# Kernel tuning notes

Hardware: AMD Instinct MI355X
Metric: run time of the kernel (lower is better)

## Reference

```python
import jax, jax.numpy as jnp
import numpy as np

DIM = 768
HEADS = 12
HEAD_DIM = DIM // HEADS
SCALE = HEAD_DIM ** (-0.5)


def setup_inputs() -> dict:
    key = jax.random.key(0)
    k1, k2, k3 = jax.random.split(key, 3)
    x = jax.random.normal(k1, (4, 2048, DIM), dtype=jnp.float32)
    # nn.Linear(dim, 3*dim, bias=False): weight [3*dim, dim]
    w_qkv = jax.random.normal(k2, (3 * DIM, DIM), dtype=jnp.float32) * (DIM ** -0.5)
    # nn.Linear(dim, dim) with bias
    w_proj = jax.random.normal(k3, (DIM, DIM), dtype=jnp.float32) * (DIM ** -0.5)
    b_proj = jnp.zeros((DIM,), dtype=jnp.float32)
    return {"x": x, "w_qkv": w_qkv, "w_proj": w_proj, "b_proj": b_proj}


def reference(x, w_qkv, w_proj, b_proj):
    B, N, C = x.shape
    H, D = HEADS, HEAD_DIM
    qkv = jnp.einsum('bnc,oc->bno', x, w_qkv)  # [B,N,3C]
    qkv = qkv.reshape(B, N, 3, H, D).transpose(2, 0, 3, 1, 4)  # [3,B,H,N,D]
    q, k, v = qkv[0], qkv[1], qkv[2]
    attn = jnp.einsum('bhnd,bhmd->bhnm', q, k) * SCALE  # [B,H,N,N]
    attn = jax.nn.softmax(attn, axis=-1)
    attn = jax.nn.softmax(attn, axis=-1)  # double softmax, as in original
    out = jnp.einsum('bhnm,bhmd->bhnd', attn, v)  # [B,H,N,D]
    out = out.transpose(0, 2, 1, 3).reshape(B, N, C)
    return jnp.einsum('bnc,oc->bno', out, w_proj) + b_proj
```

## Files before the change

### kernel.cpp

```cpp
#include <hip/hip_runtime.h>
#include <hip/hip_bf16.h>

#define DIM 768
#define HEADS 12
#define HD 64
#define SEQ 2048
#define BATCH 4
#define BHN 48
#define TOK 8192

#if __has_builtin(__builtin_amdgcn_exp2f)
#define EXP2F __builtin_amdgcn_exp2f
#else
#define EXP2F exp2f
#endif
#define EXP_C 0.1803368801111244f

using short8  = __attribute__((ext_vector_type(8))) short;
using short4v = __attribute__((ext_vector_type(4))) short;
using float4v = __attribute__((ext_vector_type(4))) float;

__device__ __forceinline__ short f2b(float f) {
    union { float f; unsigned u; } v; v.f = f;
    unsigned r = v.u + 0x7FFF + ((v.u >> 16) & 1);
    return (short)(r >> 16);
}
__device__ __forceinline__ float b2f(short s) {
    union { unsigned u; float f; } v;
    v.u = ((unsigned)(unsigned short)s) << 16;
    return v.f;
}
__device__ __forceinline__ unsigned pk2(float a, float b) {
    union { float f; unsigned u; } x, y; x.f = a; y.f = b;
    return __builtin_amdgcn_perm(x.u + 0x8000u, y.u + 0x8000u, 0x03020706u);
}

typedef const __attribute__((address_space(1))) unsigned GU;
typedef __attribute__((address_space(3))) unsigned LU;
__device__ __forceinline__ void gload_lds16(const short* g, short* l) {
    __builtin_amdgcn_global_load_lds((GU*)g, (LU*)l, 16, 0, 0);
}

__global__ void cast_all(const float* __restrict__ x, const float* __restrict__ wq,
                         const float* __restrict__ wp,
                         short* __restrict__ xb, short* __restrict__ wqb,
                         short* __restrict__ wpb, float* __restrict__ Vsum,
                         int nx4, int nq4) {
    int i = blockIdx.x * 256 + threadIdx.x;
    if (i < BHN * 64) Vsum[i] = 0.f;
    const float* in; short* out; int j = i;
    if (i < nx4)            { in = x;  out = xb;  }
    else if (i < nx4 + nq4) { in = wq; out = wqb; j = i - nx4; }
    else                    { in = wp; out = wpb; j = i - nx4 - nq4; }
    float4 f = ((const float4*)in)[j];
    short4 o;
    o.x = f2b(f.x); o.y = f2b(f.y); o.z = f2b(f.z); o.w = f2b(f.w);
    ((short4*)out)[j] = o;
}

__global__ __launch_bounds__(256, 4)
void gemm_qkv(const short* __restrict__ A, const short* __restrict__ Bw,
              short* __restrict__ Qw, short* __restrict__ Kw, short* __restrict__ Vw,
              float* __restrict__ Vsum)
{
    __shared__ __align__(16) short As[2][128 * 32];
    __shared__ __align__(16) short Bs[2][128 * 32];

    const int tid  = threadIdx.x;
    const int lane = tid & 63;
    const int wave = tid >> 6;
    const int wm = (wave >> 1) * 64, wn = (wave & 1) * 64;
    const int l15 = lane & 15, quad = lane >> 4;

    const int gid = blockIdx.x;
    const int w   = gid >> 3;
    const int ybl = (gid & 7) * 8 + (w & 7);
    const int xbl = w >> 3;

    const bool vpart = (xbl >= 12);
    const short* rowsP = vpart ? (Bw + 1536 * 768) : A;
    const short* colsP = vpart ? A : Bw;
    const int m0 = vpart ? (xbl - 12) * 128 : ybl * 128;
    const int n0 = vpart ? ybl * 128 : xbl * 128;
    const int K = DIM;

    float4v acc[4][4];
    #pragma unroll
    for (int i = 0; i < 4; i++)
        #pragma unroll
        for (int j = 0; j < 4; j++)
            acc[i][j] = (float4v){0.f, 0.f, 0.f, 0.f};

    const int G0 = wave * 128 + lane;
    const int G1 = G0 + 64;
    const int rA0 = G0 >> 2, cA0 = (G0 & 3) * 8;
    const int rA1 = G1 >> 2, cA1 = (G1 & 3) * 8;
    const int ldsoff = wave * 1024;

    for (int kt = 0; kt < K; kt += 64) {
        #pragma unroll
        for (int s = 0; s < 2; s++) {
            const int kc = kt + s * 32;
            gload_lds16(&rowsP[(size_t)(m0 + rA0) * K + kc + cA0], &As[s][ldsoff]);
            gload_lds16(&rowsP[(size_t)(m0 + rA1) * K + kc + cA1], &As[s][ldsoff + 512]);
            gload_lds16(&colsP[(size_t)(n0 + rA0) * K + kc + cA0], &Bs[s][ldsoff]);
            gload_lds16(&colsP[(size_t)(n0 + rA1) * K + kc + cA1], &Bs[s][ldsoff + 512]);
        }
        __syncthreads();
        #pragma unroll
        for (int s = 0; s < 2; s++) {
            short8 af[4], bfr[4];
            #pragma unroll
            for (int t = 0; t < 4; t++) {
                af[t]  = *(const short8*)&As[s][(wm + t * 16 + l15) * 32 + quad * 8];
                bfr[t] = *(const short8*)&Bs[s][(wn + t * 16 + l15) * 32 + quad * 8];
            }
            #pragma unroll
            for (int tm = 0; tm < 4; tm++)
                #pragma unroll
                for (int tn = 0; tn < 4; tn++)
                    acc[tm][tn] = __builtin_amdgcn_mfma_f32_16x16x32_bf16(af[tm], bfr[tn], acc[tm][tn], 0, 0, 0);
        }
        __syncthreads();
    }

    #pragma unroll
    for (int tm = 0; tm < 4; tm++)
        #pragma unroll
        for (int tn = 0; tn < 4; tn++)
            #pragma unroll
            for (int r = 0; r < 4; r++) {
                int row = m0 + wm + tm * 16 + quad * 4 + r;
                int col = n0 + wn + tn * 16 + l15;
                float v = acc[tm][tn][r];
                if (vpart) {
                    int hh = row >> 6, d = row & 63;
                    int b = col >> 11, n = col & 2047;
                    int bh = b * HEADS + hh;
                    int t2 = n >> 6, c2h = (n >> 5) & 1, wk = n & 31;
                    int slot = ((wk & 15) >> 2) * 8 + ((wk & 16) >> 2) + (wk & 3);
                    int g2 = c2h * 4 + (slot >> 3);
                    int gp2 = g2 ^ (d & 7);
                    Vw[(size_t)bh * (SEQ * 64) + t2 * 4096 + d * 64 + gp2 * 8 + (slot & 7)] = f2b(v);
                } else {
                    int hh = (col & 767) >> 6, d = col & 63;
                    int b = row >> 11, n = row & 2047;
                    int bh = b * HEADS + hh;
                    size_t idx = (size_t)bh * (SEQ * 64) + (size_t)n * 64
                               + (((d >> 3) ^ (n & 7)) << 3) + (d & 7);
                    if (col < 768) Qw[idx] = f2b(v * EXP_C);
                    else           Kw[idx] = f2b(v);
                }
            }

    if (vpart) {
        const int bb = n0 >> 11;
        #pragma unroll
        for (int tm = 0; tm < 4; tm++)
            #pragma unroll
            for (int r = 0; r < 4; r++) {
                float s4 = (acc[tm][0][r] + acc[tm][1][r]) + (acc[tm][2][r] + acc[tm][3][r]);
                #pragma unroll
                for (int m = 1; m < 16; m <<= 1) s4 += __shfl_xor(s4, m, 64);
                if (l15 == 0) {
                    int row = m0 + wm + tm * 16 + quad * 4 + r;
                    int hh = row >> 6, d = row & 63;
                    atomicAdd(&Vsum[(bb * HEADS + hh) * 64 + d], s4);
                }
            }
    }
}

__global__ __launch_bounds__(256, 4)
void gemm_proj(const short* __restrict__ A, const short* __restrict__ Bw,
               const float* __restrict__ bias, float* __restrict__ Out)
{
    __shared__ __align__(16) short As[3][128 * 32];
    __shared__ __align__(16) short Bs[3][64 * 32];

    const int tid  = threadIdx.x;
    const int lane = tid & 63;
    const int wave = tid >> 6;
    const int wm = (wave >> 1) * 64, wn = (wave & 1) * 32;
    const int l15 = lane & 15, quad = lane >> 4;

    const int gid = blockIdx.x;
    const int w   = gid >> 3;
    const int ybl = (gid & 7) * 8 + (w & 7);
    const int xbl = w >> 3;
    const int m0 = ybl * 128, n0 = xbl * 64;
    const int K = DIM;

    float4v acc[4][2];
    #pragma unroll
    for (int i = 0; i < 4; i++)
        #pragma unroll
        for (int j = 0; j < 2; j++)
            acc[i][j] = (float4v){0.f, 0.f, 0.f, 0.f};

    const int GA0 = wave * 128 + lane, GA1 = GA0 + 64;
    const int rA0 = GA0 >> 2, cA0 = (GA0 & 3) * 8;
    const int rA1 = GA1 >> 2, cA1 = (GA1 & 3) * 8;
    const int GB0 = wave * 64 + lane;
    const int rB0 = GB0 >> 2, cB0 = (GB0 & 3) * 8;
    const int ldsoffA = wave * 1024, ldsoffB = wave * 512;

    auto STAGE = [&](int t, int buf) {
        const int kc = t * 32;
        gload_lds16(&A [(size_t)(m0 + rA0) * K + kc + cA0], &As[buf][ldsoffA]);
        gload_lds16(&A [(size_t)(m0 + rA1) * K + kc + cA1], &As[buf][ldsoffA + 512]);
        gload_lds16(&Bw[(size_t)(n0 + rB0) * K + kc + cB0], &Bs[buf][ldsoffB]);
    };

    STAGE(0, 0);
    STAGE(1, 1);

    int cur = 0, nx2 = 2;
    for (int t = 0; t < 24; t++) {
        if (t < 23) { asm volatile("s_waitcnt vmcnt(3)" ::: "memory"); }
        else        { asm volatile("s_waitcnt vmcnt(0)" ::: "memory"); }
        __builtin_amdgcn_sched_barrier(0);
        __builtin_amdgcn_s_barrier();
        __builtin_amdgcn_sched_barrier(0);

        short8 af[4], bfr[2];
        #pragma unroll
        for (int tt = 0; tt < 4; tt++)
            af[tt] = *(const short8*)&As[cur][(wm + tt * 16 + l15) * 32 + quad * 8];
        #pragma unroll
        for (int tt = 0; tt < 2; tt++)
            bfr[tt] = *(const short8*)&Bs[cur][(wn + tt * 16 + l15) * 32 + quad * 8];
        #pragma unroll
        for (int tm = 0; tm < 4; tm++)
            #pragma unroll
            for (int tn = 0; tn < 2; tn++)
                acc[tm][tn] = __builtin_amdgcn_mfma_f32_16x16x32_bf16(af[tm], bfr[tn], acc[tm][tn], 0, 0, 0);

        if (t < 22) STAGE(t + 2, nx2);
        cur = (cur == 2) ? 0 : cur + 1;
        nx2 = (nx2 == 2) ? 0 : nx2 + 1;
    }

    #pragma unroll
    for (int tm = 0; tm < 4; tm++)
        #pragma unroll
        for (int tn = 0; tn < 2; tn++)
            #pragma unroll
            for (int r = 0; r < 4; r++) {
                int row = m0 + wm + tm * 16 + quad * 4 + r;
                int col = n0 + wn + tn * 16 + l15;
                Out[(size_t)row * 768 + col] = acc[tm][tn][r] + bias[col];
            }
}

__global__ __launch_bounds__(256, 3)
void attn_kernel(const short* __restrict__ Qw, const short* __restrict__ Kw,
                 const short* __restrict__ Vw, const float* __restrict__ Vsum,
                 short* __restrict__ Ow)
{
    __shared__ __align__(16) short LDS[24576];

    const int tid  = threadIdx.x;
    const int lane = tid & 63, wave = tid >> 6;
    const int l15 = lane & 15, quad = lane >> 4;
    const int r7  = l15 & 7;
    const int bid = blockIdx.x;
    const int ii  = bid >> 3;
    const int bh  = (bid & 7) * 6 + (ii >> 4);
    const int qt  = ii & 15;
    const int wq  = wave * 32;

    const short* Qp = Qw + (size_t)bh * (SEQ * 64) + qt * 8192;
    const short* Kp = Kw + (size_t)bh * (SEQ * 64);
    const short* Vp = Vw + (size_t)bh * (SEQ * 64);

    short8 onesf;
    #pragma unroll
    for (int j = 0; j < 8; j++) onesf[j] = (l15 == 0) ? (short)0x3F80 : (short)0;

    #pragma unroll
    for (int h = 0; h < 4; h++) {
        const int g = wave * 4 + h;
        gload_lds16(&Qp[g * 512 + lane * 8], &LDS[g * 512]);
    }
    __syncthreads();
    short8 aq[2][2];
    #pragma unroll
    for (int nb = 0; nb < 2; nb++)
        #pragma unroll
        for (int kk = 0; kk < 2; kk++) {
            int r = wq + nb * 16 + l15;
            aq[nb][kk] = *(const short8*)&LDS[r * 64 + (((kk * 4 + quad) ^ r7) << 3)];
        }
    __syncthreads();

    float4v Aacc[2][4], Lacc[2];
    #pragma unroll
    for (int mb = 0; mb < 2; mb++) {
        Lacc[mb] = (float4v){0.f, 0.f, 0.f, 0.f};
        #pragma unroll
        for (int t = 0; t < 4; t++) Aacc[mb][t] = (float4v){0.f, 0.f, 0.f, 0.f};
    }

    auto STAGE = [&](int t2, int kbuf) {
        const int kb = kbuf * 4096;
        #pragma unroll
        for (int h = 0; h < 2; h++) {
            const int g = wave * 2 + h;
            gload_lds16(&Kp[(size_t)t2 * 4096 + g * 512 + lane * 8], &LDS[kb + g * 512]);
            gload_lds16(&Vp[(size_t)t2 * 4096 + g * 512 + lane * 8], &LDS[12288 + kb + g * 512]);
        }
    };

    STAGE(0, 0);
    STAGE(1, 1);

    const int wodd = wave & 1;

    int cur = 0, nx2 = 2;
    for (int kt = 0; kt < 32; kt++) {
        if (kt < 31) { asm volatile("s_waitcnt vmcnt(4)" ::: "memory"); }
        else         { asm volatile("s_waitcnt vmcnt(0)" ::: "memory"); }
        __builtin_amdgcn_sched_barrier(0);
        __builtin_amdgcn_s_barrier();
        __builtin_amdgcn_sched_barrier(0);

        const short* KB = &LDS[cur * 4096];
        const short* VB = &LDS[12288 + cur * 4096];

        #pragma unroll
        for (int cc = 0; cc < 2; cc++) {
            const int c2 = cc ^ wodd;
            union AE { unsigned u[4]; short8 s; };
            AE ae[2];
            #pragma unroll
            for (int tn2 = 0; tn2 < 2; tn2++) {
                const int row = (c2 * 2 + tn2) * 16 + l15;
                const short* rp = &KB[row * 64];
                short8 b0 = *(const short8*)&rp[(quad ^ r7) << 3];
                short8 b1 = *(const short8*)&rp[((4 + quad) ^ r7) << 3];
                #pragma unroll
                for (int nb = 0; nb < 2; nb++) {
                    float4v s = (float4v){0.f, 0.f, 0.f, 0.f};
                    s = __builtin_amdgcn_mfma_f32_16x16x32_bf16(b0, aq[nb][0], s, 0, 0, 0);
                    s = __builtin_amdgcn_mfma_f32_16x16x32_bf16(b1, aq[nb][1], s, 0, 0, 0);
                    ae[nb].u[tn2 * 2]     = pk2(EXP2F(s[0]), EXP2F(s[1]));
                    ae[nb].u[tn2 * 2 + 1] = pk2(EXP2F(s[2]), EXP2F(s[3]));
                }
            }
            __builtin_amdgcn_s_setprio(1);
            Lacc[0] = __builtin_amdgcn_mfma_f32_16x16x32_bf16(ae[0].s, onesf, Lacc[0], 0, 0, 0);
            Lacc[1] = __builtin_amdgcn_mfma_f32_16x16x32_bf16(ae[1].s, onesf, Lacc[1], 0, 0, 0);
            #pragma unroll
            for (int tn = 0; tn < 4; tn++) {
                const int d = tn * 16 + l15;
                short8 bv = *(const short8*)&VB[d * 64 + (((c2 * 4 + quad) ^ r7) << 3)];
                Aacc[0][tn] = __builtin_amdgcn_mfma_f32_16x16x32_bf16(ae[0].s, bv, Aacc[0][tn], 0, 0, 0);
                Aacc[1][tn] = __builtin_amdgcn_mfma_f32_16x16x32_bf16(ae[1].s, bv, Aacc[1][tn], 0, 0, 0);
            }
            __builtin_amdgcn_s_setprio(0);
        }

        if (kt < 30) STAGE(kt + 2, nx2);
        cur = (cur == 2) ? 0 : cur + 1;
        nx2 = (nx2 == 2) ? 0 : nx2 + 1;
    }

    const int b = bh / HEADS, hh = bh - (bh / HEADS) * HEADS;
    #pragma unroll
    for (int mb = 0; mb < 2; mb++)
        #pragma unroll
        for (int r = 0; r < 4; r++) {
            float il = 1.f / __shfl(Lacc[mb][r], lane & 48, 64);
            int row = qt * 128 + wq + mb * 16 + quad * 4 + r;
            int tok = b * SEQ + row;
            #pragma unroll
            for (int tn = 0; tn < 4; tn++) {
                int d = tn * 16 + l15;
                float vs = Vsum[bh * 64 + d];
                float val = (vs + Aacc[mb][tn][r] * il) * (1.f / 2049.f);
                Ow[(size_t)tok * 768 + hh * 64 + d] = f2b(val);
            }
        }
}

extern "C" void kernel_launch(void* const* d_in, const int* in_sizes, int n_in,
                              void* d_out, int out_size, void* d_ws, size_t ws_size,
                              hipStream_t stream) {
    const float* x      = (const float*)d_in[0];
    const float* w_qkv  = (const float*)d_in[1];
    const float* w_proj = (const float*)d_in[2];
    const float* b_proj = (const float*)d_in[3];
    float* out = (float*)d_out;

    char* ws = (char*)d_ws;
    size_t off = 0;
    auto alloc = [&](size_t bytes) {
        void* p = ws + off;
        off += (bytes + 255) & ~(size_t)255;
        return p;
    };
    short* x_bf  = (short*)alloc((size_t)TOK * DIM * 2);
    short* wq_bf = (short*)alloc((size_t)3 * DIM * DIM * 2);
    short* wp_bf = (short*)alloc((size_t)DIM * DIM * 2);
    short* Qw    = (short*)alloc((size_t)BHN * SEQ * 64 * 2);
    short* Kw    = (short*)alloc((size_t)BHN * SEQ * 64 * 2);
    short* Vw    = (short*)alloc((size_t)BHN * SEQ * 64 * 2);
    short* Ow    = (short*)alloc((size_t)TOK * DIM * 2);
    float* Vsum  = (float*)alloc((size_t)BHN * 64 * 4);

    int nx4 = TOK * DIM / 4, nq4 = 3 * DIM * DIM / 4, np4 = DIM * DIM / 4;
    int tot4 = nx4 + nq4 + np4;
    cast_all<<<tot4 / 256, 256, 0, stream>>>(x, w_qkv, w_proj, x_bf, wq_bf, wp_bf, Vsum, nx4, nq4);

    gemm_qkv<<<1152, 256, 0, stream>>>(x_bf, wq_bf, Qw, Kw, Vw, Vsum);

    attn_kernel<<<BHN * 16, 256, 0, stream>>>(Qw, Kw, Vw, Vsum, Ow);

    gemm_proj<<<768, 256, 0, stream>>>(Ow, wp_bf, b_proj, out);
}
```

Before: 201.5 us.

## Stage QKV GEMM epilogue through LDS for coalesced 16-byte stores

The QKV GEMM epilogue used to write scattered 2-byte bf16 values straight to global memory in the swizzled Q/K/V layouts. It now writes the swizzled tile into shared memory, which is enlarged and padded, then copies it out with coalesced short8 stores per head and tile. This is meant to cut uncoalesced global write traffic, at the cost of extra LDS space and a barrier that may lower occupancy. Separately, the attention kernel drops the per-wave alternation of the c2 chunk order.

Result: no change. 200.3 us (-0.6%).

```diff
diff --git a/kernel.cpp b/kernel.cpp
--- a/kernel.cpp
+++ b/kernel.cpp
@@ -63,8 +63,9 @@
               short* __restrict__ Qw, short* __restrict__ Kw, short* __restrict__ Vw,
               float* __restrict__ Vsum)
 {
-    __shared__ __align__(16) short As[2][128 * 32];
-    __shared__ __align__(16) short Bs[2][128 * 32];
+    __shared__ __align__(16) short SMEM[18432];
+    short* As = SMEM;
+    short* Bs = SMEM + 8192;
 
     const int tid  = threadIdx.x;
     const int lane = tid & 63;
@@ -101,10 +102,10 @@
         #pragma unroll
         for (int s = 0; s < 2; s++) {
             const int kc = kt + s * 32;
-            gload_lds16(&rowsP[(size_t)(m0 + rA0) * K + kc + cA0], &As[s][ldsoff]);
-            gload_lds16(&rowsP[(size_t)(m0 + rA1) * K + kc + cA1], &As[s][ldsoff + 512]);
-            gload_lds16(&colsP[(size_t)(n0 + rA0) * K + kc + cA0], &Bs[s][ldsoff]);
-            gload_lds16(&colsP[(size_t)(n0 + rA1) * K + kc + cA1], &Bs[s][ldsoff + 512]);
+            gload_lds16(&rowsP[(size_t)(m0 + rA0) * K + kc + cA0], &As[s * 4096 + ldsoff]);
+            gload_lds16(&rowsP[(size_t)(m0 + rA1) * K + kc + cA1], &As[s * 4096 + ldsoff + 512]);
+            gload_lds16(&colsP[(size_t)(n0 + rA0) * K + kc + cA0], &Bs[s * 4096 + ldsoff]);
+            gload_lds16(&colsP[(size_t)(n0 + rA1) * K + kc + cA1], &Bs[s * 4096 + ldsoff + 512]);
         }
         __syncthreads();
         #pragma unroll
@@ -112,8 +113,8 @@
             short8 af[4], bfr[4];
             #pragma unroll
             for (int t = 0; t < 4; t++) {
-                af[t]  = *(const short8*)&As[s][(wm + t * 16 + l15) * 32 + quad * 8];
-                bfr[t] = *(const short8*)&Bs[s][(wn + t * 16 + l15) * 32 + quad * 8];
+                af[t]  = *(const short8*)&As[s * 4096 + (wm + t * 16 + l15) * 32 + quad * 8];
+                bfr[t] = *(const short8*)&Bs[s * 4096 + (wn + t * 16 + l15) * 32 + quad * 8];
             }
             #pragma unroll
             for (int tm = 0; tm < 4; tm++)
@@ -124,37 +125,64 @@
         __syncthreads();
     }
 
-    #pragma unroll
-    for (int tm = 0; tm < 4; tm++)
-        #pragma unroll
-        for (int tn = 0; tn < 4; tn++)
-            #pragma unroll
-            for (int r = 0; r < 4; r++) {
-                int row = m0 + wm + tm * 16 + quad * 4 + r;
-                int col = n0 + wn + tn * 16 + l15;
-                float v = acc[tm][tn][r];
-                if (vpart) {
-                    int hh = row >> 6, d = row & 63;
-                    int b = col >> 11, n = col & 2047;
-                    int bh = b * HEADS + hh;
-                    int t2 = n >> 6, c2h = (n >> 5) & 1, wk = n & 31;
-                    int slot = ((wk & 15) >> 2) * 8 + ((wk & 16) >> 2) + (wk & 3);
-                    int g2 = c2h * 4 + (slot >> 3);
-                    int gp2 = g2 ^ (d & 7);
-                    Vw[(size_t)bh * (SEQ * 64) + t2 * 4096 + d * 64 + gp2 * 8 + (slot & 7)] = f2b(v);
-                } else {
-                    int hh = (col & 767) >> 6, d = col & 63;
-                    int b = row >> 11, n = row & 2047;
-                    int bh = b * HEADS + hh;
-                    size_t idx = (size_t)bh * (SEQ * 64) + (size_t)n * 64
-                               + (((d >> 3) ^ (n & 7)) << 3) + (d & 7);
-                    if (col < 768) Qw[idx] = f2b(v * EXP_C);
-                    else           Kw[idx] = f2b(v);
+    if (!vpart) {
+        const int g = wave & 1;
+        #pragma unroll
+        for (int tm = 0; tm < 4; tm++)
+            #pragma unroll
+            for (int tn = 0; tn < 4; tn++)
+                #pragma unroll
+                for (int r = 0; r < 4; r++) {
+                    int lr = wm + tm * 16 + quad * 4 + r;
+                    int d  = tn * 16 + l15;
+                    float v = acc[tm][tn][r];
+                    short o = (xbl < 6) ? f2b(v * EXP_C) : f2b(v);
+                    SMEM[lr * 136 + g * 64 + (((d >> 3) ^ (lr & 7)) << 3) + (d & 7)] = o;
                 }
-            }
-
-    if (vpart) {
-        const int bb = n0 >> 11;
+        __syncthreads();
+        short* base = (xbl < 6) ? Qw : Kw;
+        const int hh0 = ((xbl < 6) ? xbl : xbl - 6) * 2;
+        const int b = m0 >> 11;
+        #pragma unroll
+        for (int g2 = 0; g2 < 2; g2++) {
+            short* dst = base + ((size_t)(b * HEADS + hh0 + g2)) * (SEQ * 64);
+            #pragma unroll
+            for (int it = 0; it < 4; it++) {
+                int lr = it * 32 + (tid >> 3);
+                short8 vv = *(const short8*)&SMEM[lr * 136 + g2 * 64 + (tid & 7) * 8];
+                *(short8*)&dst[(size_t)(m0 + lr) * 64 + (tid & 7) * 8] = vv;
+            }
+        }
+    } else {
+        const int g  = wave >> 1;
+        const int th = wave & 1;
+        #pragma unroll
+        for (int tm = 0; tm < 4; tm++)
+            #pragma unroll
+            for (int tn = 0; tn < 4; tn++)
+                #pragma unroll
+                for (int r = 0; r < 4; r++) {
+                    int d = tm * 16 + quad * 4 + r;
+                    int g2v = (tn >> 1) * 4 + (l15 >> 2);
+                    int gp2 = g2v ^ (d & 7);
+                    int off = (gp2 << 3) + ((tn & 1) << 2) + (l15 & 3);
+                    SMEM[(g * 2 + th) * 4608 + d * 72 + off] = f2b(acc[tm][tn][r]);
+                }
+        __syncthreads();
+        const int b2 = n0 >> 11;
+        #pragma unroll
+        for (int reg = 0; reg < 4; reg++) {
+            int gg = reg >> 1, t2h = reg & 1;
+            int hh = (xbl - 12) * 2 + gg;
+            short* dst = Vw + ((size_t)(b2 * HEADS + hh)) * (SEQ * 64)
+                            + (size_t)((n0 >> 6) + t2h) * 4096;
+            #pragma unroll
+            for (int it = 0; it < 2; it++) {
+                int d = it * 32 + (tid >> 3);
+                short8 vv = *(const short8*)&SMEM[reg * 4608 + d * 72 + (tid & 7) * 8];
+                *(short8*)&dst[d * 64 + (tid & 7) * 8] = vv;
+            }
+        }
         #pragma unroll
         for (int tm = 0; tm < 4; tm++)
             #pragma unroll
@@ -165,7 +193,7 @@
                 if (l15 == 0) {
                     int row = m0 + wm + tm * 16 + quad * 4 + r;
                     int hh = row >> 6, d = row & 63;
-                    atomicAdd(&Vsum[(bb * HEADS + hh) * 64 + d], s4);
+                    atomicAdd(&Vsum[(b2 * HEADS + hh) * 64 + d], s4);
                 }
             }
     }
@@ -315,8 +343,6 @@
     STAGE(0, 0);
     STAGE(1, 1);
 
-    const int wodd = wave & 1;
-
     int cur = 0, nx2 = 2;
     for (int kt = 0; kt < 32; kt++) {
         if (kt < 31) { asm volatile("s_waitcnt vmcnt(4)" ::: "memory"); }
@@ -329,8 +355,7 @@
         const short* VB = &LDS[12288 + cur * 4096];
 
         #pragma unroll
-        for (int cc = 0; cc < 2; cc++) {
-            const int c2 = cc ^ wodd;
+        for (int c2 = 0; c2 < 2; c2++) {
             union AE { unsigned u[4]; short8 s; };
             AE ae[2];
             #pragma unroll
```
